# Kernel optimization log

Hardware: AMD Instinct MI355X
Metric: run time of the kernel (lower is better)

Reference implementation:

```python
import jax, jax.numpy as jnp
import numpy as np

B, T = 4096, 2048
CLIP = 1.0e5


def _hv(x):
    # smooth Heaviside: ~0 for x<0, ~1 for x>0
    return (jnp.tanh(5.0 * x) + 1.0) * 0.5


def setup_inputs() -> dict:
    key = jax.random.key(0)
    k1, _ = jax.random.split(key)
    # columns: prcp, tmean, dayl (all in [0,1) like normalized forcings)
    inputs = jax.random.uniform(k1, (B, T, 3), dtype=jnp.float32)
    # 15 scalar bucket parameters, all initialized to 0.5 as in build():
    # f, smax, qmax, ddf, tmin, tmax, Kc, SCmax, spmax, qpmax, kp, sgmax, qgmax, Kl, Kn
    theta = jnp.full((15,), 0.5, dtype=jnp.float32)
    return {"inputs": inputs, "theta": theta}


def _run(inputs, theta):
    f, smax, qmax, ddf, tmin, tmax, Kc, SCmax, spmax, qpmax, kp, sgmax, qgmax, Kl, Kn = [
        theta[i] for i in range(15)
    ]
    prcp = inputs[:, :, 0]   # [B,T]
    tmean = inputs[:, :, 1]
    dayl = inputs[:, :, 2]
    # Hamon-style PET computed once for the whole sequence
    pet = 29.8 * (dayl * 24.0) * 0.611 * jnp.exp(17.3 * tmean / (tmean + 237.3)) / (tmean + 273.2)

    # rescaled parameters (done once; constant over time)
    f_ = f / 10.0
    smax_ = smax * 1950.0
    qmax_ = qmax * 50.0
    ddf_ = ddf * 5.0
    tmin_ = tmin * -3.0
    tmax_ = tmax * 3.0
    Kc_ = Kc * 0.5
    SCmax_ = SCmax * 1.5
    spmax_ = spmax * 1950.0
    qpmax_ = qpmax * 40.0
    sgmax_ = sgmax * 1950.0
    qgmax_ = qgmax * 40.0
    Kl_ = Kl * 0.5
    Kn_ = Kn * 0.5
    Dc = 0.986 * 0.862

    def step(state, xt):
        s0, s1, s2, s3, s4 = [state[:, i] for i in range(5)]  # each [B]
        p, t, dl, pe = xt  # each [B]

        # canopy bucket
        day = _hv(dl - 0.5)
        night = _hv(0.5 - dl)
        scmax_t = day * SCmax_ * 2.0 + night * SCmax_ * 0.6
        lai_t = day * 0.478 + night * 0.15
        kc_t = day * Kc_ + night * Kc_ * 0.4
        pintc = (_hv(p - 0.1) * _hv(s0) * _hv(s0 - scmax_t) * p
                 + _hv(p - 0.1) * _hv(scmax_t - s0) * kc_t * Dc * lai_t)

        # rain/snow partition
        psnow = _hv(tmin_ - t) * p
        prain = _hv(t - tmin_) * p

        # snow bucket
        melt = _hv(t - tmax_) * _hv(s1) * jnp.minimum(s1, ddf_ * (t - tmax_))

        # preferential bucket
        qpref = (_hv(s2) * _hv(s2 - spmax_) * qpmax_
                 + _hv(s2) * _hv(spmax_ - s2) * kp * p * jnp.exp(-f_ * (spmax_ - s2)))

        # capillary (soil) bucket
        et = (_hv(s3) * _hv(s3 - smax_) * pe
              + _hv(s3) * _hv(smax_ - s3) * pe * (s3 / smax_))
        qsub = (_hv(s3) * _hv(s3 - smax_) * qmax_
                + _hv(s3) * _hv(smax_ - s3) * qmax_ * jnp.exp(-f_ * (smax_ - s3)))
        qout = _hv(s3) * _hv(s3 - smax_) * (s3 - smax_)

        # gravity bucket
        qslow = (_hv(s4) * _hv(s4 - sgmax_) * qgmax_
                 + _hv(s4) * _hv(sgmax_ - s4) * (p * Kl_ + p * p * Kn_) * jnp.exp(-f_ * (sgmax_ - s4)))

        ns0 = s0 + jnp.clip(pintc, -CLIP, CLIP)
        ns1 = s1 + jnp.clip(psnow - melt, -CLIP, CLIP)
        ns2 = s2 + jnp.clip(qpref, -CLIP, CLIP)
        ns3 = s3 + jnp.clip(prain + melt - et - qsub - qout, -CLIP, CLIP)
        ns4 = s4 + jnp.clip(qslow, -CLIP, CLIP)
        new_state = jnp.stack([ns0, ns1, ns2, ns3, ns4], axis=1)  # [B,5]
        return new_state, new_state

    init = jnp.zeros((inputs.shape[0], 5), dtype=inputs.dtype)
    xs = (prcp.T, tmean.T, dayl.T, pet.T)  # time-major [T,B]
    _, seq = jax.lax.scan(step, init, xs)  # seq: [T,B,5]
    return jnp.transpose(seq, (1, 0, 2))  # [B,T,5] state trajectories


def reference(inputs, theta):
    return _run(inputs, theta)
```

## Files before the change

### kernel.cpp

```cpp
#include <hip/hip_runtime.h>


#define NB 4096
#define NT 2048
#define CHUNK 16
#define NCHUNK (NT / CHUNK)
#define BT ((size_t)NB * (size_t)NT)

#define L2E10 14.4269504089f
#define L2E    1.44269504089f

__device__ __forceinline__ float rcpf(float x) { return __builtin_amdgcn_rcpf(x); }
__device__ __forceinline__ float ex2(float a)  { return __builtin_amdgcn_exp2f(a); }
__device__ __forceinline__ float ex2c(float a) { return __builtin_amdgcn_exp2f(fminf(a, 80.0f)); }
__device__ __forceinline__ float clip1e5(float x) {
    return __builtin_amdgcn_fmed3f(x, -100000.0f, 100000.0f);
}

__global__ __launch_bounds__(64, 1)
void prnn_roles(const float* __restrict__ inp, const float* __restrict__ theta,
                float* __restrict__ out, float* __restrict__ wsp, int use_ws) {
    const int lane = threadIdx.x;
    const int role = blockIdx.x & 3;
    const int b = (blockIdx.x >> 2) * 64 + lane;

    const float f_     = theta[0] * 0.1f;
    const float smax_  = theta[1] * 1950.0f;
    const float qmax_  = theta[2] * 50.0f;
    const float ddf_   = theta[3] * 5.0f;
    const float tmin_  = theta[4] * -3.0f;
    const float tmax_  = theta[5] * 3.0f;
    const float Kc_    = theta[6] * 0.5f;
    const float SCmax_ = theta[7] * 1.5f;
    const float spmax_ = theta[8] * 1950.0f;
    const float qpmax_ = theta[9] * 40.0f;
    const float kp     = theta[10];
    const float sgmax_ = theta[11] * 1950.0f;
    const float qgmax_ = theta[12] * 40.0f;
    const float Kl_    = theta[13] * 0.5f;
    const float Kn_    = theta[14] * 0.5f;

    const float inv_smax = rcpf(smax_);
    const float KcDc  = Kc_ * 0.849932f;
    const float c_sn  = -L2E10 * tmin_;
    const float c_m   =  L2E10 * tmax_;
    const float c_dd  = -ddf_ * tmax_;
    const float c_sc1 =  L2E10 * SCmax_ * 1.4f;
    const float c_sc0 =  L2E10 * SCmax_ * 0.6f;
    const float c_2p  =  L2E10 * spmax_;
    const float c_3s  =  L2E10 * smax_;
    const float c_4s  =  L2E10 * sgmax_;
    const float fE    = f_ * L2E;
    const float c_E2  = -fE * spmax_;
    const float c_E3  = -fE * smax_;
    const float c_E4  = -fE * sgmax_;

    const float* ip = inp + (size_t)b * (NT * 3);
    float*       op = out + (size_t)b * (NT * 5);
    float* wbase = use_ws ? wsp : out;

    auto plane_store = [&](float* plane, const float* ob, int c) {
        float4* d = (float4*)(plane + (size_t)c * CHUNK);
        const float4* s = (const float4*)ob;
        #pragma unroll
        for (int i = 0; i < CHUNK / 4; ++i) d[i] = s[i];
    };

    if (role == 0) {
        float s0 = 0.f;
        float bA[CHUNK * 3], bB[CHUNK * 3];
        float* w0 = wbase + 0 * BT + (size_t)b * NT;
        auto pf = [&](float* d, int c) {
            const float4* s = (const float4*)(ip + (size_t)c * (CHUNK * 3));
            #pragma unroll
            for (int i = 0; i < (CHUNK * 3) / 4; ++i) ((float4*)d)[i] = s[i];
        };
        auto cw = [&](const float* d, int c) {
            float ob[CHUNK];
            #pragma unroll
            for (int i = 0; i < CHUNK; ++i) {
                const float p  = d[i * 3 + 0];
                const float dl = d[i * 3 + 2];
                const float day = rcpf(1.0f + ex2(fmaf(-L2E10, dl, 7.21347520f)));
                const float da  = 1.0f + ex2(fmaf(-L2E10, p, L2E));
                const float lai   = fmaf(0.328f, day, 0.15f);
                const float kcf   = fmaf(0.6f, day, 0.4f);
                const float kterm = KcDc * kcf * lai;
                const float zday  = fmaf(c_sc1, day, c_sc0);
                const float e0  = ex2(-L2E10 * s0);
                const float esc = ex2(fmaf(-L2E10, s0, zday));
                const float d0  = 1.0f + e0;
                const float dsc = 1.0f + esc;
                const float Rp  = rcpf(da * d0 * dsc);
                const float pintc = Rp * fmaf(d0 * esc, kterm, p);
                s0 += clip1e5(pintc);
                ob[i] = s0;
            }
            if (use_ws) plane_store(w0, ob, c);
            else {
                #pragma unroll
                for (int i = 0; i < CHUNK; ++i) op[(c * CHUNK + i) * 5 + 0] = ob[i];
            }
        };
        pf(bA, 0);
        for (int c = 0; c < NCHUNK; c += 2) {
            pf(bB, c + 1);
            cw(bA, c);
            if (c + 2 < NCHUNK) pf(bA, c + 2);
            cw(bB, c + 1);
        }
    } else if (role == 1) {
        float s1 = 0.f, s3 = 0.f;
        float bA[CHUNK * 3], bB[CHUNK * 3];
        float* w1 = wbase + 1 * BT + (size_t)b * NT;
        float* w3 = wbase + 3 * BT + (size_t)b * NT;
        auto pf = [&](float* d, int c) {
            const float4* s = (const float4*)(ip + (size_t)c * (CHUNK * 3));
            #pragma unroll
            for (int i = 0; i < (CHUNK * 3) / 4; ++i) ((float4*)d)[i] = s[i];
        };
        auto cw = [&](const float* d, int c) {
            float ob1[CHUNK], ob3[CHUNK];
            #pragma unroll
            for (int i = 0; i < CHUNK; ++i) {
                const float p  = d[i * 3 + 0];
                const float tm = d[i * 3 + 1];
                const float dl = d[i * 3 + 2];
                const float A1 = tm + 237.3f;
                const float A2 = tm + 273.2f;
                const float q  = rcpf(A1 * A2);
                const float pe = 436.98672f * dl * ex2(24.958624f * tm * (q * A2)) * (q * A1);
                const float psnow = rcpf(1.0f + ex2(fmaf(L2E10, tm, c_sn))) * p;
                const float dm = 1.0f + ex2(fmaf(-L2E10, tm, c_m));
                const float prain = p - psnow;
                const float e1 = ex2(-L2E10 * s1);
                const float melt = rcpf(dm * (1.0f + e1))
                                   * fminf(s1, fmaf(ddf_, tm, c_dd));
                const float e3  = ex2(-L2E10 * s3);
                const float e3s = ex2c(fmaf(-L2E10, s3, c_3s));
                const float R3  = rcpf((1.0f + e3) * (1.0f + e3s));
                const float E3  = ex2(fmaf(fE, s3, c_E3));
                const float t_et = pe * fmaf(e3s * s3, inv_smax, 1.0f);
                const float t_qs = qmax_ * fmaf(e3s, E3, 1.0f);
                const float outflux = R3 * (t_et + t_qs + (s3 - smax_));
                const float ds3 = prain + melt - outflux;
                s1 += clip1e5(psnow - melt);
                s3 += clip1e5(ds3);
                ob1[i] = s1;
                ob3[i] = s3;
            }
            if (use_ws) { plane_store(w1, ob1, c); plane_store(w3, ob3, c); }
            else {
                #pragma unroll
                for (int i = 0; i < CHUNK; ++i) {
                    op[(c * CHUNK + i) * 5 + 1] = ob1[i];
                    op[(c * CHUNK + i) * 5 + 3] = ob3[i];
                }
            }
        };
        pf(bA, 0);
        for (int c = 0; c < NCHUNK; c += 2) {
            pf(bB, c + 1);
            cw(bA, c);
            if (c + 2 < NCHUNK) pf(bA, c + 2);
            cw(bB, c + 1);
        }
    } else if (role == 2) {
        float s2 = 0.f;
        float pA[CHUNK], pB[CHUNK];
        float* w2 = wbase + 2 * BT + (size_t)b * NT;
        auto pf = [&](float* P, int c) {
            #pragma unroll
            for (int i = 0; i < CHUNK; ++i) P[i] = ip[(c * CHUNK + i) * 3 + 0];
        };
        auto cw = [&](const float* P, int c) {
            float ob[CHUNK];
            #pragma unroll
            for (int i = 0; i < CHUNK; ++i) {
                const float p = P[i];
                const float e2  = ex2(-L2E10 * s2);
                const float e2p = ex2c(fmaf(-L2E10, s2, c_2p));
                const float R2  = rcpf((1.0f + e2) * (1.0f + e2p));
                const float E2  = ex2(fmaf(fE, s2, c_E2));
                const float qpref = R2 * fmaf(e2p * E2, kp * p, qpmax_);
                s2 += clip1e5(qpref);
                ob[i] = s2;
            }
            if (use_ws) plane_store(w2, ob, c);
            else {
                #pragma unroll
                for (int i = 0; i < CHUNK; ++i) op[(c * CHUNK + i) * 5 + 2] = ob[i];
            }
        };
        pf(pA, 0);
        for (int c = 0; c < NCHUNK; c += 2) {
            pf(pB, c + 1);
            cw(pA, c);
            if (c + 2 < NCHUNK) pf(pA, c + 2);
            cw(pB, c + 1);
        }
    } else {
        float s4 = 0.f;
        float pA[CHUNK], pB[CHUNK];
        float* w4 = wbase + 4 * BT + (size_t)b * NT;
        auto pf = [&](float* P, int c) {
            #pragma unroll
            for (int i = 0; i < CHUNK; ++i) P[i] = ip[(c * CHUNK + i) * 3 + 0];
        };
        auto cw = [&](const float* P, int c) {
            float ob[CHUNK];
            #pragma unroll
            for (int i = 0; i < CHUNK; ++i) {
                const float p = P[i];
                const float e4  = ex2(-L2E10 * s4);
                const float e4s = ex2c(fmaf(-L2E10, s4, c_4s));
                const float R4  = rcpf((1.0f + e4) * (1.0f + e4s));
                const float E4  = ex2(fmaf(fE, s4, c_E4));
                const float pl  = p * fmaf(p, Kn_, Kl_);
                const float qslow = R4 * fmaf(e4s * E4, pl, qgmax_);
                s4 += clip1e5(qslow);
                ob[i] = s4;
            }
            if (use_ws) plane_store(w4, ob, c);
            else {
                #pragma unroll
                for (int i = 0; i < CHUNK; ++i) op[(c * CHUNK + i) * 5 + 4] = ob[i];
            }
        };
        pf(pA, 0);
        for (int c = 0; c < NCHUNK; c += 2) {
            pf(pB, c + 1);
            cw(pA, c);
            if (c + 2 < NCHUNK) pf(pA, c + 2);
            cw(pB, c + 1);
        }
    }
}

__global__ __launch_bounds__(256)
void tx_kernel(const float* __restrict__ wsp, float* __restrict__ out) {
    const size_t idx = (size_t)blockIdx.x * 256 + threadIdx.x;
    const size_t b  = idx / (NT / 4);
    const size_t t0 = (idx % (NT / 4)) * 4;
    const float* base = wsp + b * NT + t0;
    const float4 v0 = *(const float4*)(base + 0 * BT);
    const float4 v1 = *(const float4*)(base + 1 * BT);
    const float4 v2 = *(const float4*)(base + 2 * BT);
    const float4 v3 = *(const float4*)(base + 3 * BT);
    const float4 v4 = *(const float4*)(base + 4 * BT);
    float4* o = (float4*)(out + (b * NT + t0) * 5);
    o[0] = make_float4(v0.x, v1.x, v2.x, v3.x);
    o[1] = make_float4(v4.x, v0.y, v1.y, v2.y);
    o[2] = make_float4(v3.y, v4.y, v0.z, v1.z);
    o[3] = make_float4(v2.z, v3.z, v4.z, v0.w);
    o[4] = make_float4(v1.w, v2.w, v3.w, v4.w);
}

extern "C" void kernel_launch(void* const* d_in, const int* in_sizes, int n_in,
                              void* d_out, int out_size, void* d_ws, size_t ws_size,
                              hipStream_t stream) {
    const float* inp   = (const float*)d_in[0];
    const float* theta = (const float*)d_in[1];
    float* out = (float*)d_out;
    float* wsp = (float*)d_ws;
    const int use_ws = (wsp != nullptr && ws_size >= 5 * sizeof(float) * BT) ? 1 : 0;
    prnn_roles<<<4 * (NB / 64), 64, 0, stream>>>(inp, theta, out, wsp, use_ws);
    if (use_ws)
        tx_kernel<<<(int)(BT / 4 / 256), 256, 0, stream>>>(wsp, out);
}
```

Before: 559.4 us.

## Interleave two independent batch rows per thread to hide recurrence latency

Each thread now advances two independent batch rows in an interleaved way, giving the serial per-timestep dependency chain (exp/rcp latency) instruction-level parallelism. The grid is halved from 256 to 128 blocks and CHUNK is reduced to 8 to keep register use comparable. The risk is that only 128 single-wave blocks run on a GPU with many more CUs, which cuts parallelism across the chip, and the smaller chunks mean smaller prefetch batches.

```diff
diff --git a/kernel.cpp b/kernel.cpp
--- a/kernel.cpp
+++ b/kernel.cpp
@@ -3,7 +3,7 @@
 
 #define NB 4096
 #define NT 2048
-#define CHUNK 16
+#define CHUNK 8
 #define NCHUNK (NT / CHUNK)
 #define BT ((size_t)NB * (size_t)NT)
 
@@ -22,7 +22,8 @@
                 float* __restrict__ out, float* __restrict__ wsp, int use_ws) {
     const int lane = threadIdx.x;
     const int role = blockIdx.x & 3;
-    const int b = (blockIdx.x >> 2) * 64 + lane;
+    const int b0 = (blockIdx.x >> 2) * 128 + lane;
+    const int b1 = b0 + 64;
 
     const float f_     = theta[0] * 0.1f;
     const float smax_  = theta[1] * 1950.0f;
@@ -55,8 +56,10 @@
     const float c_E3  = -fE * smax_;
     const float c_E4  = -fE * sgmax_;
 
-    const float* ip = inp + (size_t)b * (NT * 3);
-    float*       op = out + (size_t)b * (NT * 5);
+    const float* ip0 = inp + (size_t)b0 * (NT * 3);
+    const float* ip1 = inp + (size_t)b1 * (NT * 3);
+    float*       op0 = out + (size_t)b0 * (NT * 5);
+    float*       op1 = out + (size_t)b1 * (NT * 5);
     float* wbase = use_ws ? wsp : out;
 
     auto plane_store = [&](float* plane, const float* ob, int c) {
@@ -67,172 +70,278 @@
     };
 
     if (role == 0) {
-        float s0 = 0.f;
-        float bA[CHUNK * 3], bB[CHUNK * 3];
-        float* w0 = wbase + 0 * BT + (size_t)b * NT;
-        auto pf = [&](float* d, int c) {
-            const float4* s = (const float4*)(ip + (size_t)c * (CHUNK * 3));
-            #pragma unroll
-            for (int i = 0; i < (CHUNK * 3) / 4; ++i) ((float4*)d)[i] = s[i];
-        };
-        auto cw = [&](const float* d, int c) {
-            float ob[CHUNK];
-            #pragma unroll
-            for (int i = 0; i < CHUNK; ++i) {
-                const float p  = d[i * 3 + 0];
-                const float dl = d[i * 3 + 2];
-                const float day = rcpf(1.0f + ex2(fmaf(-L2E10, dl, 7.21347520f)));
-                const float da  = 1.0f + ex2(fmaf(-L2E10, p, L2E));
-                const float lai   = fmaf(0.328f, day, 0.15f);
-                const float kcf   = fmaf(0.6f, day, 0.4f);
-                const float kterm = KcDc * kcf * lai;
-                const float zday  = fmaf(c_sc1, day, c_sc0);
-                const float e0  = ex2(-L2E10 * s0);
-                const float esc = ex2(fmaf(-L2E10, s0, zday));
-                const float d0  = 1.0f + e0;
-                const float dsc = 1.0f + esc;
-                const float Rp  = rcpf(da * d0 * dsc);
-                const float pintc = Rp * fmaf(d0 * esc, kterm, p);
-                s0 += clip1e5(pintc);
-                ob[i] = s0;
-            }
-            if (use_ws) plane_store(w0, ob, c);
-            else {
-                #pragma unroll
-                for (int i = 0; i < CHUNK; ++i) op[(c * CHUNK + i) * 5 + 0] = ob[i];
-            }
-        };
-        pf(bA, 0);
-        for (int c = 0; c < NCHUNK; c += 2) {
-            pf(bB, c + 1);
-            cw(bA, c);
-            if (c + 2 < NCHUNK) pf(bA, c + 2);
-            cw(bB, c + 1);
-        }
-    } else if (role == 1) {
-        float s1 = 0.f, s3 = 0.f;
-        float bA[CHUNK * 3], bB[CHUNK * 3];
-        float* w1 = wbase + 1 * BT + (size_t)b * NT;
-        float* w3 = wbase + 3 * BT + (size_t)b * NT;
-        auto pf = [&](float* d, int c) {
-            const float4* s = (const float4*)(ip + (size_t)c * (CHUNK * 3));
-            #pragma unroll
-            for (int i = 0; i < (CHUNK * 3) / 4; ++i) ((float4*)d)[i] = s[i];
-        };
-        auto cw = [&](const float* d, int c) {
-            float ob1[CHUNK], ob3[CHUNK];
-            #pragma unroll
-            for (int i = 0; i < CHUNK; ++i) {
-                const float p  = d[i * 3 + 0];
-                const float tm = d[i * 3 + 1];
-                const float dl = d[i * 3 + 2];
-                const float A1 = tm + 237.3f;
-                const float A2 = tm + 273.2f;
-                const float q  = rcpf(A1 * A2);
-                const float pe = 436.98672f * dl * ex2(24.958624f * tm * (q * A2)) * (q * A1);
-                const float psnow = rcpf(1.0f + ex2(fmaf(L2E10, tm, c_sn))) * p;
-                const float dm = 1.0f + ex2(fmaf(-L2E10, tm, c_m));
-                const float prain = p - psnow;
-                const float e1 = ex2(-L2E10 * s1);
-                const float melt = rcpf(dm * (1.0f + e1))
-                                   * fminf(s1, fmaf(ddf_, tm, c_dd));
-                const float e3  = ex2(-L2E10 * s3);
-                const float e3s = ex2c(fmaf(-L2E10, s3, c_3s));
-                const float R3  = rcpf((1.0f + e3) * (1.0f + e3s));
-                const float E3  = ex2(fmaf(fE, s3, c_E3));
-                const float t_et = pe * fmaf(e3s * s3, inv_smax, 1.0f);
-                const float t_qs = qmax_ * fmaf(e3s, E3, 1.0f);
-                const float outflux = R3 * (t_et + t_qs + (s3 - smax_));
-                const float ds3 = prain + melt - outflux;
-                s1 += clip1e5(psnow - melt);
-                s3 += clip1e5(ds3);
-                ob1[i] = s1;
-                ob3[i] = s3;
-            }
-            if (use_ws) { plane_store(w1, ob1, c); plane_store(w3, ob3, c); }
+        float sA = 0.f, sB = 0.f;
+        float a0[CHUNK * 3], a1[CHUNK * 3], q0[CHUNK * 3], q1[CHUNK * 3];
+        float* w0a = wbase + 0 * BT + (size_t)b0 * NT;
+        float* w0b = wbase + 0 * BT + (size_t)b1 * NT;
+        auto pf = [&](float* d0, float* d1, int c) {
+            const float4* s0 = (const float4*)(ip0 + (size_t)c * (CHUNK * 3));
+            const float4* s1 = (const float4*)(ip1 + (size_t)c * (CHUNK * 3));
+            #pragma unroll
+            for (int i = 0; i < (CHUNK * 3) / 4; ++i) {
+                ((float4*)d0)[i] = s0[i];
+                ((float4*)d1)[i] = s1[i];
+            }
+        };
+        auto cw = [&](const float* d0, const float* d1, int c) {
+            float ob0[CHUNK], ob1[CHUNK];
+            #pragma unroll
+            for (int i = 0; i < CHUNK; ++i) {
+                {
+                    const float p  = d0[i * 3 + 0];
+                    const float dl = d0[i * 3 + 2];
+                    const float day = rcpf(1.0f + ex2(fmaf(-L2E10, dl, 7.21347520f)));
+                    const float da  = 1.0f + ex2(fmaf(-L2E10, p, L2E));
+                    const float lai   = fmaf(0.328f, day, 0.15f);
+                    const float kcf   = fmaf(0.6f, day, 0.4f);
+                    const float kterm = KcDc * kcf * lai;
+                    const float zday  = fmaf(c_sc1, day, c_sc0);
+                    const float e0  = ex2(-L2E10 * sA);
+                    const float esc = ex2(fmaf(-L2E10, sA, zday));
+                    const float d0_ = 1.0f + e0;
+                    const float dsc = 1.0f + esc;
+                    const float Rp  = rcpf(da * d0_ * dsc);
+                    const float pintc = Rp * fmaf(d0_ * esc, kterm, p);
+                    sA += clip1e5(pintc);
+                    ob0[i] = sA;
+                }
+                {
+                    const float p  = d1[i * 3 + 0];
+                    const float dl = d1[i * 3 + 2];
+                    const float day = rcpf(1.0f + ex2(fmaf(-L2E10, dl, 7.21347520f)));
+                    const float da  = 1.0f + ex2(fmaf(-L2E10, p, L2E));
+                    const float lai   = fmaf(0.328f, day, 0.15f);
+                    const float kcf   = fmaf(0.6f, day, 0.4f);
+                    const float kterm = KcDc * kcf * lai;
+                    const float zday  = fmaf(c_sc1, day, c_sc0);
+                    const float e0  = ex2(-L2E10 * sB);
+                    const float esc = ex2(fmaf(-L2E10, sB, zday));
+                    const float d0_ = 1.0f + e0;
+                    const float dsc = 1.0f + esc;
+                    const float Rp  = rcpf(da * d0_ * dsc);
+                    const float pintc = Rp * fmaf(d0_ * esc, kterm, p);
+                    sB += clip1e5(pintc);
+                    ob1[i] = sB;
+                }
+            }
+            if (use_ws) { plane_store(w0a, ob0, c); plane_store(w0b, ob1, c); }
             else {
                 #pragma unroll
                 for (int i = 0; i < CHUNK; ++i) {
-                    op[(c * CHUNK + i) * 5 + 1] = ob1[i];
-                    op[(c * CHUNK + i) * 5 + 3] = ob3[i];
-                }
-            }
-        };
-        pf(bA, 0);
+                    op0[(c * CHUNK + i) * 5 + 0] = ob0[i];
+                    op1[(c * CHUNK + i) * 5 + 0] = ob1[i];
+                }
+            }
+        };
+        pf(a0, a1, 0);
         for (int c = 0; c < NCHUNK; c += 2) {
-            pf(bB, c + 1);
-            cw(bA, c);
-            if (c + 2 < NCHUNK) pf(bA, c + 2);
-            cw(bB, c + 1);
+            pf(q0, q1, c + 1);
+            cw(a0, a1, c);
+            if (c + 2 < NCHUNK) pf(a0, a1, c + 2);
+            cw(q0, q1, c + 1);
+        }
+    } else if (role == 1) {
+        float s1A = 0.f, s3A = 0.f, s1B = 0.f, s3B = 0.f;
+        float a0[CHUNK * 3], a1[CHUNK * 3], q0[CHUNK * 3], q1[CHUNK * 3];
+        float* w1a = wbase + 1 * BT + (size_t)b0 * NT;
+        float* w1b = wbase + 1 * BT + (size_t)b1 * NT;
+        float* w3a = wbase + 3 * BT + (size_t)b0 * NT;
+        float* w3b = wbase + 3 * BT + (size_t)b1 * NT;
+        auto pf = [&](float* d0, float* d1, int c) {
+            const float4* s0 = (const float4*)(ip0 + (size_t)c * (CHUNK * 3));
+            const float4* s1 = (const float4*)(ip1 + (size_t)c * (CHUNK * 3));
+            #pragma unroll
+            for (int i = 0; i < (CHUNK * 3) / 4; ++i) {
+                ((float4*)d0)[i] = s0[i];
+                ((float4*)d1)[i] = s1[i];
+            }
+        };
+        auto cw = [&](const float* d0, const float* d1, int c) {
+            float ob1a[CHUNK], ob3a[CHUNK], ob1b[CHUNK], ob3b[CHUNK];
+            #pragma unroll
+            for (int i = 0; i < CHUNK; ++i) {
+                {
+                    const float p  = d0[i * 3 + 0];
+                    const float tm = d0[i * 3 + 1];
+                    const float dl = d0[i * 3 + 2];
+                    const float A1 = tm + 237.3f;
+                    const float A2 = tm + 273.2f;
+                    const float qq = rcpf(A1 * A2);
+                    const float pe = 436.98672f * dl * ex2(24.958624f * tm * (qq * A2)) * (qq * A1);
+                    const float psnow = rcpf(1.0f + ex2(fmaf(L2E10, tm, c_sn))) * p;
+                    const float dm = 1.0f + ex2(fmaf(-L2E10, tm, c_m));
+                    const float prain = p - psnow;
+                    const float e1 = ex2(-L2E10 * s1A);
+                    const float melt = rcpf(dm * (1.0f + e1))
+                                       * fminf(s1A, fmaf(ddf_, tm, c_dd));
+                    const float e3  = ex2(-L2E10 * s3A);
+                    const float e3s = ex2c(fmaf(-L2E10, s3A, c_3s));
+                    const float R3  = rcpf((1.0f + e3) * (1.0f + e3s));
+                    const float E3  = ex2(fmaf(fE, s3A, c_E3));
+                    const float t_et = pe * fmaf(e3s * s3A, inv_smax, 1.0f);
+                    const float t_qs = qmax_ * fmaf(e3s, E3, 1.0f);
+                    const float outflux = R3 * (t_et + t_qs + (s3A - smax_));
+                    const float ds3 = prain + melt - outflux;
+                    s1A += clip1e5(psnow - melt);
+                    s3A += clip1e5(ds3);
+                    ob1a[i] = s1A;
+                    ob3a[i] = s3A;
+                }
+                {
+                    const float p  = d1[i * 3 + 0];
+                    const float tm = d1[i * 3 + 1];
+                    const float dl = d1[i * 3 + 2];
+                    const float A1 = tm + 237.3f;
+                    const float A2 = tm + 273.2f;
+                    const float qq = rcpf(A1 * A2);
+                    const float pe = 436.98672f * dl * ex2(24.958624f * tm * (qq * A2)) * (qq * A1);
+                    const float psnow = rcpf(1.0f + ex2(fmaf(L2E10, tm, c_sn))) * p;
+                    const float dm = 1.0f + ex2(fmaf(-L2E10, tm, c_m));
+                    const float prain = p - psnow;
+                    const float e1 = ex2(-L2E10 * s1B);
+                    const float melt = rcpf(dm * (1.0f + e1))
+                                       * fminf(s1B, fmaf(ddf_, tm, c_dd));
+                    const float e3  = ex2(-L2E10 * s3B);
+                    const float e3s = ex2c(fmaf(-L2E10, s3B, c_3s));
+                    const float R3  = rcpf((1.0f + e3) * (1.0f + e3s));
+                    const float E3  = ex2(fmaf(fE, s3B, c_E3));
+                    const float t_et = pe * fmaf(e3s * s3B, inv_smax, 1.0f);
+                    const float t_qs = qmax_ * fmaf(e3s, E3, 1.0f);
+                    const float outflux = R3 * (t_et + t_qs + (s3B - smax_));
+                    const float ds3 = prain + melt - outflux;
+                    s1B += clip1e5(psnow - melt);
+                    s3B += clip1e5(ds3);
+                    ob1b[i] = s1B;
+                    ob3b[i] = s3B;
+                }
+            }
+            if (use_ws) {
+                plane_store(w1a, ob1a, c); plane_store(w3a, ob3a, c);
+                plane_store(w1b, ob1b, c); plane_store(w3b, ob3b, c);
+            } else {
+                #pragma unroll
+                for (int i = 0; i < CHUNK; ++i) {
+                    op0[(c * CHUNK + i) * 5 + 1] = ob1a[i];
+                    op0[(c * CHUNK + i) * 5 + 3] = ob3a[i];
+                    op1[(c * CHUNK + i) * 5 + 1] = ob1b[i];
+                    op1[(c * CHUNK + i) * 5 + 3] = ob3b[i];
+                }
+            }
+        };
+        pf(a0, a1, 0);
+        for (int c = 0; c < NCHUNK; c += 2) {
+            pf(q0, q1, c + 1);
+            cw(a0, a1, c);
+            if (c + 2 < NCHUNK) pf(a0, a1, c + 2);
+            cw(q0, q1, c + 1);
         }
     } else if (role == 2) {
-        float s2 = 0.f;
-        float pA[CHUNK], pB[CHUNK];
-        float* w2 = wbase + 2 * BT + (size_t)b * NT;
-        auto pf = [&](float* P, int c) {
-            #pragma unroll
-            for (int i = 0; i < CHUNK; ++i) P[i] = ip[(c * CHUNK + i) * 3 + 0];
-        };
-        auto cw = [&](const float* P, int c) {
-            float ob[CHUNK];
-            #pragma unroll
-            for (int i = 0; i < CHUNK; ++i) {
-                const float p = P[i];
-                const float e2  = ex2(-L2E10 * s2);
-                const float e2p = ex2c(fmaf(-L2E10, s2, c_2p));
-                const float R2  = rcpf((1.0f + e2) * (1.0f + e2p));
-                const float E2  = ex2(fmaf(fE, s2, c_E2));
-                const float qpref = R2 * fmaf(e2p * E2, kp * p, qpmax_);
-                s2 += clip1e5(qpref);
-                ob[i] = s2;
-            }
-            if (use_ws) plane_store(w2, ob, c);
+        float sA = 0.f, sB = 0.f;
+        float a0[CHUNK], a1[CHUNK], q0[CHUNK], q1[CHUNK];
+        float* w2a = wbase + 2 * BT + (size_t)b0 * NT;
+        float* w2b = wbase + 2 * BT + (size_t)b1 * NT;
+        auto pf = [&](float* P0, float* P1, int c) {
+            #pragma unroll
+            for (int i = 0; i < CHUNK; ++i) {
+                P0[i] = ip0[(c * CHUNK + i) * 3 + 0];
+                P1[i] = ip1[(c * CHUNK + i) * 3 + 0];
+            }
+        };
+        auto cw = [&](const float* P0, const float* P1, int c) {
+            float ob0[CHUNK], ob1[CHUNK];
+            #pragma unroll
+            for (int i = 0; i < CHUNK; ++i) {
+                {
+                    const float p = P0[i];
+                    const float e2  = ex2(-L2E10 * sA);
+                    const float e2p = ex2c(fmaf(-L2E10, sA, c_2p));
+                    const float R2  = rcpf((1.0f + e2) * (1.0f + e2p));
+                    const float E2  = ex2(fmaf(fE, sA, c_E2));
+                    const float qpref = R2 * fmaf(e2p * E2, kp * p, qpmax_);
+                    sA += clip1e5(qpref);
+                    ob0[i] = sA;
+                }
+                {
+                    const float p = P1[i];
+                    const float e2  = ex2(-L2E10 * sB);
+                    const float e2p = ex2c(fmaf(-L2E10, sB, c_2p));
+                    const float R2  = rcpf((1.0f + e2) * (1.0f + e2p));
+                    const float E2  = ex2(fmaf(fE, sB, c_E2));
+                    const float qpref = R2 * fmaf(e2p * E2, kp * p, qpmax_);
+                    sB += clip1e5(qpref);
+                    ob1[i] = sB;
+                }
+            }
+            if (use_ws) { plane_store(w2a, ob0, c); plane_store(w2b, ob1, c); }
             else {
                 #pragma unroll
-                for (int i = 0; i < CHUNK; ++i) op[(c * CHUNK + i) * 5 + 2] = ob[i];
-            }
-        };
-        pf(pA, 0);
+                for (int i = 0; i < CHUNK; ++i) {
+                    op0[(c * CHUNK + i) * 5 + 2] = ob0[i];
+                    op1[(c * CHUNK + i) * 5 + 2] = ob1[i];
+                }
+            }
+        };
+        pf(a0, a1, 0);
         for (int c = 0; c < NCHUNK; c += 2) {
-            pf(pB, c + 1);
-            cw(pA, c);
-            if (c + 2 < NCHUNK) pf(pA, c + 2);
-            cw(pB, c + 1);
+            pf(q0, q1, c + 1);
+            cw(a0, a1, c);
+            if (c + 2 < NCHUNK) pf(a0, a1, c + 2);
+            cw(q0, q1, c + 1);
         }
     } else {
-        float s4 = 0.f;
-        float pA[CHUNK], pB[CHUNK];
-        float* w4 = wbase + 4 * BT + (size_t)b * NT;
-        auto pf = [&](float* P, int c) {
-            #pragma unroll
-            for (int i = 0; i < CHUNK; ++i) P[i] = ip[(c * CHUNK + i) * 3 + 0];
-        };
-        auto cw = [&](const float* P, int c) {
-            float ob[CHUNK];
-            #pragma unroll
-            for (int i = 0; i < CHUNK; ++i) {
-                const float p = P[i];
-                const float e4  = ex2(-L2E10 * s4);
-                const float e4s = ex2c(fmaf(-L2E10, s4, c_4s));
-                const float R4  = rcpf((1.0f + e4) * (1.0f + e4s));
-                const float E4  = ex2(fmaf(fE, s4, c_E4));
-                const float pl  = p * fmaf(p, Kn_, Kl_);
-                const float qslow = R4 * fmaf(e4s * E4, pl, qgmax_);
-                s4 += clip1e5(qslow);
-                ob[i] = s4;
-            }
-            if (use_ws) plane_store(w4, ob, c);
+        float sA = 0.f, sB = 0.f;
+        float a0[CHUNK], a1[CHUNK], q0[CHUNK], q1[CHUNK];
+        float* w4a = wbase + 4 * BT + (size_t)b0 * NT;
+        float* w4b = wbase + 4 * BT + (size_t)b1 * NT;
+        auto pf = [&](float* P0, float* P1, int c) {
+            #pragma unroll
+            for (int i = 0; i < CHUNK; ++i) {
+                P0[i] = ip0[(c * CHUNK + i) * 3 + 0];
+                P1[i] = ip1[(c * CHUNK + i) * 3 + 0];
+            }
+        };
+        auto cw = [&](const float* P0, const float* P1, int c) {
+            float ob0[CHUNK], ob1[CHUNK];
+            #pragma unroll
+            for (int i = 0; i < CHUNK; ++i) {
+                {
+                    const float p = P0[i];
+                    const float e4  = ex2(-L2E10 * sA);
+                    const float e4s = ex2c(fmaf(-L2E10, sA, c_4s));
+                    const float R4  = rcpf((1.0f + e4) * (1.0f + e4s));
+                    const float E4  = ex2(fmaf(fE, sA, c_E4));
+                    const float pl  = p * fmaf(p, Kn_, Kl_);
+                    const float qslow = R4 * fmaf(e4s * E4, pl, qgmax_);
+                    sA += clip1e5(qslow);
+                    ob0[i] = sA;
+                }
+                {
+                    const float p = P1[i];
+                    const float e4  = ex2(-L2E10 * sB);
+                    const float e4s = ex2c(fmaf(-L2E10, sB, c_4s));
+                    const float R4  = rcpf((1.0f + e4) * (1.0f + e4s));
+                    const float E4  = ex2(fmaf(fE, sB, c_E4));
+                    const float pl  = p * fmaf(p, Kn_, Kl_);
+                    const float qslow = R4 * fmaf(e4s * E4, pl, qgmax_);
+                    sB += clip1e5(qslow);
+                    ob1[i] = sB;
+                }
+            }
+            if (use_ws) { plane_store(w4a, ob0, c); plane_store(w4b, ob1, c); }
             else {
                 #pragma unroll
-                for (int i = 0; i < CHUNK; ++i) op[(c * CHUNK + i) * 5 + 4] = ob[i];
-            }
-        };
-        pf(pA, 0);
+                for (int i = 0; i < CHUNK; ++i) {
+                    op0[(c * CHUNK + i) * 5 + 4] = ob0[i];
+                    op1[(c * CHUNK + i) * 5 + 4] = ob1[i];
+                }
+            }
+        };
+        pf(a0, a1, 0);
         for (int c = 0; c < NCHUNK; c += 2) {
-            pf(pB, c + 1);
-            cw(pA, c);
-            if (c + 2 < NCHUNK) pf(pA, c + 2);
-            cw(pB, c + 1);
+            pf(q0, q1, c + 1);
+            cw(a0, a1, c);
+            if (c + 2 < NCHUNK) pf(a0, a1, c + 2);
+            cw(q0, q1, c + 1);
         }
     }
 }
@@ -264,7 +373,7 @@
     float* out = (float*)d_out;
     float* wsp = (float*)d_ws;
     const int use_ws = (wsp != nullptr && ws_size >= 5 * sizeof(float) * BT) ? 1 : 0;
-    prnn_roles<<<4 * (NB / 64), 64, 0, stream>>>(inp, theta, out, wsp, use_ws);
+    prnn_roles<<<4 * (NB / 128), 64, 0, stream>>>(inp, theta, out, wsp, use_ws);
     if (use_ws)
         tx_kernel<<<(int)(BT / 4 / 256), 256, 0, stream>>>(wsp, out);
 }
```

Result: slower. 857.4 us (+53.3%).

## Precompute time-independent forcing terms in a separate kernel for the snow/soil role

Applied to the files above, without the earlier changes.

Adds a pre-pass kernel that computes PET, snow/rain partition, melt denominator and degree-day melt for every (b,t) and writes them as planes into the output buffer used as scratch. The role-1 recurrence, which handles s1 and s3, then reads these five planes instead of recomputing the exp/rcp work inside its serial loop, shortening the critical path of the slowest role. In exchange it adds a full extra pass that reads and writes about 5*B*T floats, plus an extra kernel launch. Output is later overwritten by the transpose kernel.

```diff
diff --git a/kernel.cpp b/kernel.cpp
--- a/kernel.cpp
+++ b/kernel.cpp
@@ -5,6 +5,8 @@
 #define NT 2048
 #define CHUNK 16
 #define NCHUNK (NT / CHUNK)
+#define K1 8
+#define NCH1 (NT / K1)
 #define BT ((size_t)NB * (size_t)NT)
 
 #define L2E10 14.4269504089f
@@ -15,6 +17,37 @@
 __device__ __forceinline__ float ex2c(float a) { return __builtin_amdgcn_exp2f(fminf(a, 80.0f)); }
 __device__ __forceinline__ float clip1e5(float x) {
     return __builtin_amdgcn_fmed3f(x, -100000.0f, 100000.0f);
+}
+
+__global__ __launch_bounds__(256)
+void pre_kernel(const float* __restrict__ inp, const float* __restrict__ theta,
+                float* __restrict__ scr) {
+    const float ddf_  = theta[3] * 5.0f;
+    const float tmin_ = theta[4] * -3.0f;
+    const float tmax_ = theta[5] * 3.0f;
+    const float c_sn  = -L2E10 * tmin_;
+    const float c_m   =  L2E10 * tmax_;
+    const float c_dd  = -ddf_ * tmax_;
+
+    const size_t k = (size_t)blockIdx.x * 256 + threadIdx.x;
+    const float p  = inp[k * 3 + 0];
+    const float tm = inp[k * 3 + 1];
+    const float dl = inp[k * 3 + 2];
+
+    const float A1 = tm + 237.3f;
+    const float A2 = tm + 273.2f;
+    const float q  = rcpf(A1 * A2);
+    const float pe = 436.98672f * dl * ex2(24.958624f * tm * (q * A2)) * (q * A1);
+    const float psnow = rcpf(1.0f + ex2(fmaf(L2E10, tm, c_sn))) * p;
+    const float prain = p - psnow;
+    const float dm  = 1.0f + ex2(fmaf(-L2E10, tm, c_m));
+    const float mdd = fmaf(ddf_, tm, c_dd);
+
+    scr[0 * BT + k] = pe;
+    scr[1 * BT + k] = psnow;
+    scr[2 * BT + k] = prain;
+    scr[3 * BT + k] = dm;
+    scr[4 * BT + k] = mdd;
 }
 
 __global__ __launch_bounds__(64, 1)
@@ -59,11 +92,11 @@
     float*       op = out + (size_t)b * (NT * 5);
     float* wbase = use_ws ? wsp : out;
 
-    auto plane_store = [&](float* plane, const float* ob, int c) {
-        float4* d = (float4*)(plane + (size_t)c * CHUNK);
+    auto plane_store16 = [&](float* plane, const float* ob, int off) {
+        float4* d = (float4*)(plane + (size_t)off);
         const float4* s = (const float4*)ob;
         #pragma unroll
-        for (int i = 0; i < CHUNK / 4; ++i) d[i] = s[i];
+        for (int i = 0; i < 4; ++i) d[i] = s[i];
     };
 
     if (role == 0) {
@@ -96,7 +129,7 @@
                 s0 += clip1e5(pintc);
                 ob[i] = s0;
             }
-            if (use_ws) plane_store(w0, ob, c);
+            if (use_ws) plane_store16(w0, ob, c * CHUNK);
             else {
                 #pragma unroll
                 for (int i = 0; i < CHUNK; ++i) op[(c * CHUNK + i) * 5 + 0] = ob[i];
@@ -111,59 +144,105 @@
         }
     } else if (role == 1) {
         float s1 = 0.f, s3 = 0.f;
-        float bA[CHUNK * 3], bB[CHUNK * 3];
         float* w1 = wbase + 1 * BT + (size_t)b * NT;
         float* w3 = wbase + 3 * BT + (size_t)b * NT;
-        auto pf = [&](float* d, int c) {
-            const float4* s = (const float4*)(ip + (size_t)c * (CHUNK * 3));
-            #pragma unroll
-            for (int i = 0; i < (CHUNK * 3) / 4; ++i) ((float4*)d)[i] = s[i];
-        };
-        auto cw = [&](const float* d, int c) {
-            float ob1[CHUNK], ob3[CHUNK];
-            #pragma unroll
-            for (int i = 0; i < CHUNK; ++i) {
-                const float p  = d[i * 3 + 0];
-                const float tm = d[i * 3 + 1];
-                const float dl = d[i * 3 + 2];
-                const float A1 = tm + 237.3f;
-                const float A2 = tm + 273.2f;
-                const float q  = rcpf(A1 * A2);
-                const float pe = 436.98672f * dl * ex2(24.958624f * tm * (q * A2)) * (q * A1);
-                const float psnow = rcpf(1.0f + ex2(fmaf(L2E10, tm, c_sn))) * p;
-                const float dm = 1.0f + ex2(fmaf(-L2E10, tm, c_m));
-                const float prain = p - psnow;
-                const float e1 = ex2(-L2E10 * s1);
-                const float melt = rcpf(dm * (1.0f + e1))
-                                   * fminf(s1, fmaf(ddf_, tm, c_dd));
-                const float e3  = ex2(-L2E10 * s3);
-                const float e3s = ex2c(fmaf(-L2E10, s3, c_3s));
-                const float R3  = rcpf((1.0f + e3) * (1.0f + e3s));
-                const float E3  = ex2(fmaf(fE, s3, c_E3));
-                const float t_et = pe * fmaf(e3s * s3, inv_smax, 1.0f);
-                const float t_qs = qmax_ * fmaf(e3s, E3, 1.0f);
-                const float outflux = R3 * (t_et + t_qs + (s3 - smax_));
-                const float ds3 = prain + melt - outflux;
-                s1 += clip1e5(psnow - melt);
-                s3 += clip1e5(ds3);
-                ob1[i] = s1;
-                ob3[i] = s3;
-            }
-            if (use_ws) { plane_store(w1, ob1, c); plane_store(w3, ob3, c); }
-            else {
+        if (use_ws) {
+            const float* PE = out + 0 * BT + (size_t)b * NT;
+            const float* PS = out + 1 * BT + (size_t)b * NT;
+            const float* PR = out + 2 * BT + (size_t)b * NT;
+            const float* DM = out + 3 * BT + (size_t)b * NT;
+            const float* MD = out + 4 * BT + (size_t)b * NT;
+            float peA[K1], psA[K1], prA[K1], dmA[K1], mdA[K1];
+            float peB[K1], psB[K1], prB[K1], dmB[K1], mdB[K1];
+            float ob1[2 * K1], ob3[2 * K1];
+            auto pf = [&](float* pe_, float* ps_, float* pr_, float* dm_,
+                          float* md_, int c) {
+                const int o = c * K1;
+                #pragma unroll
+                for (int i = 0; i < K1 / 4; ++i) {
+                    ((float4*)pe_)[i] = *(const float4*)(PE + o + i * 4);
+                    ((float4*)ps_)[i] = *(const float4*)(PS + o + i * 4);
+                    ((float4*)pr_)[i] = *(const float4*)(PR + o + i * 4);
+                    ((float4*)dm_)[i] = *(const float4*)(DM + o + i * 4);
+                    ((float4*)md_)[i] = *(const float4*)(MD + o + i * 4);
+                }
+            };
+            auto cw = [&](const float* pe_, const float* ps_, const float* pr_,
+                          const float* dm_, const float* md_, int half) {
+                #pragma unroll
+                for (int i = 0; i < K1; ++i) {
+                    const float pe = pe_[i], psnow = ps_[i], prain = pr_[i];
+                    const float dm = dm_[i], mdd = md_[i];
+                    const float e1 = ex2(-L2E10 * s1);
+                    const float melt = rcpf(dm * (1.0f + e1)) * fminf(s1, mdd);
+                    const float e3  = ex2(-L2E10 * s3);
+                    const float e3s = ex2c(fmaf(-L2E10, s3, c_3s));
+                    const float R3  = rcpf((1.0f + e3) * (1.0f + e3s));
+                    const float E3  = ex2(fmaf(fE, s3, c_E3));
+                    const float t_et = pe * fmaf(e3s * s3, inv_smax, 1.0f);
+                    const float t_qs = qmax_ * fmaf(e3s, E3, 1.0f);
+                    const float outflux = R3 * (t_et + t_qs + (s3 - smax_));
+                    const float ds3 = prain + melt - outflux;
+                    s1 += clip1e5(psnow - melt);
+                    s3 += clip1e5(ds3);
+                    ob1[half * K1 + i] = s1;
+                    ob3[half * K1 + i] = s3;
+                }
+            };
+            pf(peA, psA, prA, dmA, mdA, 0);
+            for (int c = 0; c < NCH1; c += 2) {
+                pf(peB, psB, prB, dmB, mdB, c + 1);
+                cw(peA, psA, prA, dmA, mdA, 0);
+                if (c + 2 < NCH1) pf(peA, psA, prA, dmA, mdA, c + 2);
+                cw(peB, psB, prB, dmB, mdB, 1);
+                plane_store16(w1, ob1, c * K1);
+                plane_store16(w3, ob3, c * K1);
+            }
+        } else {
+            float bA[CHUNK * 3], bB[CHUNK * 3];
+            auto pf = [&](float* d, int c) {
+                const float4* s = (const float4*)(ip + (size_t)c * (CHUNK * 3));
+                #pragma unroll
+                for (int i = 0; i < (CHUNK * 3) / 4; ++i) ((float4*)d)[i] = s[i];
+            };
+            auto cw = [&](const float* d, int c) {
                 #pragma unroll
                 for (int i = 0; i < CHUNK; ++i) {
-                    op[(c * CHUNK + i) * 5 + 1] = ob1[i];
-                    op[(c * CHUNK + i) * 5 + 3] = ob3[i];
+                    const float p  = d[i * 3 + 0];
+                    const float tm = d[i * 3 + 1];
+                    const float dl = d[i * 3 + 2];
+                    const float A1 = tm + 237.3f;
+                    const float A2 = tm + 273.2f;
+                    const float qq = rcpf(A1 * A2);
+                    const float pe = 436.98672f * dl * ex2(24.958624f * tm * (qq * A2)) * (qq * A1);
+                    const float psnow = rcpf(1.0f + ex2(fmaf(L2E10, tm, c_sn))) * p;
+                    const float dm = 1.0f + ex2(fmaf(-L2E10, tm, c_m));
+                    const float prain = p - psnow;
+                    const float e1 = ex2(-L2E10 * s1);
+                    const float melt = rcpf(dm * (1.0f + e1))
+                                       * fminf(s1, fmaf(ddf_, tm, c_dd));
+                    const float e3  = ex2(-L2E10 * s3);
+                    const float e3s = ex2c(fmaf(-L2E10, s3, c_3s));
+                    const float R3  = rcpf((1.0f + e3) * (1.0f + e3s));
+                    const float E3  = ex2(fmaf(fE, s3, c_E3));
+                    const float t_et = pe * fmaf(e3s * s3, inv_smax, 1.0f);
+                    const float t_qs = qmax_ * fmaf(e3s, E3, 1.0f);
+                    const float outflux = R3 * (t_et + t_qs + (s3 - smax_));
+                    const float ds3 = prain + melt - outflux;
+                    s1 += clip1e5(psnow - melt);
+                    s3 += clip1e5(ds3);
+                    const int t = c * CHUNK + i;
+                    op[t * 5 + 1] = s1;
+                    op[t * 5 + 3] = s3;
                 }
-            }
-        };
-        pf(bA, 0);
-        for (int c = 0; c < NCHUNK; c += 2) {
-            pf(bB, c + 1);
-            cw(bA, c);
-            if (c + 2 < NCHUNK) pf(bA, c + 2);
-            cw(bB, c + 1);
+            };
+            pf(bA, 0);
+            for (int c = 0; c < NCHUNK; c += 2) {
+                pf(bB, c + 1);
+                cw(bA, c);
+                if (c + 2 < NCHUNK) pf(bA, c + 2);
+                cw(bB, c + 1);
+            }
         }
     } else if (role == 2) {
         float s2 = 0.f;
@@ -186,7 +265,7 @@
                 s2 += clip1e5(qpref);
                 ob[i] = s2;
             }
-            if (use_ws) plane_store(w2, ob, c);
+            if (use_ws) plane_store16(w2, ob, c * CHUNK);
             else {
                 #pragma unroll
                 for (int i = 0; i < CHUNK; ++i) op[(c * CHUNK + i) * 5 + 2] = ob[i];
@@ -221,7 +300,7 @@
                 s4 += clip1e5(qslow);
                 ob[i] = s4;
             }
-            if (use_ws) plane_store(w4, ob, c);
+            if (use_ws) plane_store16(w4, ob, c * CHUNK);
             else {
                 #pragma unroll
                 for (int i = 0; i < CHUNK; ++i) op[(c * CHUNK + i) * 5 + 4] = ob[i];
@@ -264,6 +343,8 @@
     float* out = (float*)d_out;
     float* wsp = (float*)d_ws;
     const int use_ws = (wsp != nullptr && ws_size >= 5 * sizeof(float) * BT) ? 1 : 0;
+    if (use_ws)
+        pre_kernel<<<(int)(BT / 256), 256, 0, stream>>>(inp, theta, out);
     prnn_roles<<<4 * (NB / 64), 64, 0, stream>>>(inp, theta, out, wsp, use_ws);
     if (use_ws)
         tx_kernel<<<(int)(BT / 4 / 256), 256, 0, stream>>>(wsp, out);
```

New measurement: 617.9 us. 10.5% more time.
